# Performance work log

Hardware: AMD Instinct MI355X
Metric: run time of the kernel (lower is better)

## Reference

```python
import jax, jax.numpy as jnp
import numpy as np

EMBED_DIM = 1024
NUM_HEADS = 8
SEQ_LEN = 2048
EPS = 1e-6


def setup_inputs() -> dict:
    key = jax.random.key(0)
    ks = jax.random.split(key, 8)
    E, NH, S = EMBED_DIM, NUM_HEADS, SEQ_LEN
    q = jax.random.normal(ks[0], (S, E), jnp.float32)
    k = jax.random.normal(ks[1], (S, E), jnp.float32)
    v = jax.random.normal(ks[2], (S, E), jnp.float32)
    # gate projections: weights init'd to zeros in the module; use small random
    # values so the gate math is exercised. Biases follow the module's init.
    Wi = 0.02 * jax.random.normal(ks[3], (NH, 3 * E), jnp.float32)
    bi = jnp.linspace(3.0, 6.0, NH, dtype=jnp.float32)
    Wf = 0.02 * jax.random.normal(ks[4], (NH, 3 * E), jnp.float32)
    bf = jnp.sqrt(0.1) * jax.random.normal(ks[5], (NH,), jnp.float32)
    # ResidualLayerNorm (xLSTM-style): effective scale = 1 + weight, no bias
    ln_weight = jnp.zeros((E,), jnp.float32)
    return {"q": q, "k": k, "v": v, "Wi": Wi, "bi": bi, "Wf": Wf, "bf": bf,
            "ln_weight": ln_weight}


def _mlstm_parallel(q, k, v, Wi, bi, Wf, bf, ln_weight):
    S, E = q.shape
    NH = Wi.shape[0]
    DH = E // NH
    gate_in = jnp.concatenate((q, k, v), axis=1)            # (S, 3E)
    ig = (gate_in @ Wi.T + bi).T[:, :, None]                # (NH, S, 1)
    fg = (gate_in @ Wf.T + bf).T[:, :, None]                # (NH, S, 1)

    qh = q.reshape(S, NH, DH).transpose(1, 0, 2)            # (NH, S, DH)
    kh = k.reshape(S, NH, DH).transpose(1, 0, 2)
    vh = v.reshape(S, NH, DH).transpose(1, 0, 2)

    # cumulative log forget gates
    log_f = jax.nn.log_sigmoid(fg)                          # (NH, S, 1)
    log_f_cum = jnp.concatenate(
        [jnp.zeros((NH, 1, 1), q.dtype), jnp.cumsum(log_f, axis=1)], axis=1
    )                                                       # (NH, S+1, 1)
    log_fg_mat = log_f_cum - log_f_cum.transpose(0, 2, 1)   # (NH, S+1, S+1)
    causal = jnp.tril(jnp.ones((S, S), bool))
    log_fg_mat = jnp.where(causal, log_fg_mat[:, 1:, 1:], -jnp.inf)  # (NH,S,S)

    log_D = log_fg_mat + ig.transpose(0, 2, 1)              # (NH, S, S)
    max_log_D = jnp.max(log_D, axis=-1, keepdims=True)      # (NH, S, 1)
    D = jnp.exp(log_D - max_log_D)                          # stabilized

    qk = jnp.einsum('hsd,htd->hst', qh, kh) / jnp.sqrt(jnp.asarray(DH, q.dtype))
    C = qk * D                                              # (NH, S, S)
    normalizer = jnp.maximum(jnp.abs(jnp.sum(C, axis=-1, keepdims=True)),
                             jnp.exp(-max_log_D))
    C_norm = C / (normalizer + EPS)
    h = jnp.einsum('hst,htd->hsd', C_norm, vh)              # (NH, S, DH)
    h = h.transpose(1, 0, 2).reshape(S, E)

    # residual layer norm: LN(h) * (1 + weight), no bias
    mu = jnp.mean(h, axis=-1, keepdims=True)
    var = jnp.mean(jnp.square(h - mu), axis=-1, keepdims=True)
    h_norm = (h - mu) * jax.lax.rsqrt(var + 1e-5)
    return h_norm * (1.0 + ln_weight)


def reference(q, k, v, Wi, bi, Wf, bf, ln_weight):
    return _mlstm_parallel(q, k, v, Wi, bi, Wf, bf, ln_weight)
```

## Files before the change

kernel.cpp:

```cpp
#include <hip/hip_runtime.h>
#include <math.h>

#define S_LEN 2048
#define EMB   1024
#define NHEAD 8
#define DH    128
#define E3    3072
#define BM    64
#define BN    32
#define NSPLIT 4
#define KSTRIDE  136
#define VTSTRIDE 40
#define PTSTRIDE 40

typedef __bf16 bf16x8 __attribute__((ext_vector_type(8)));
typedef __bf16 bf16x4 __attribute__((ext_vector_type(4)));
typedef float  f32x4  __attribute__((ext_vector_type(4)));

__global__ __launch_bounds__(256) void gates_cvt_transpose_kernel(
    const float* __restrict__ q, const float* __restrict__ k,
    const float* __restrict__ v,
    const float* __restrict__ Wi, const float* __restrict__ bi,
    const float* __restrict__ Wf, const float* __restrict__ bf,
    __bf16* __restrict__ Qh, __bf16* __restrict__ Ql,
    __bf16* __restrict__ Kh, __bf16* __restrict__ Kl,
    __bf16* __restrict__ Vt,
    float* __restrict__ ig, float* __restrict__ lf)
{
    const int tid = threadIdx.x;
    __shared__ union {
        float red[16][4];
        __bf16 tile[32][33];
    } sh;

    if (blockIdx.x < S_LEN) {
        const int t = blockIdx.x;
        const float4 qv = ((const float4*)q)[(size_t)t * 256 + tid];
        const float4 kv = ((const float4*)k)[(size_t)t * 256 + tid];
        const float4 vv = ((const float4*)v)[(size_t)t * 256 + tid];
        {
            size_t idx = (size_t)t * 256 + tid;
            bf16x4 hi, lo;
            hi[0]=(__bf16)qv.x; hi[1]=(__bf16)qv.y; hi[2]=(__bf16)qv.z; hi[3]=(__bf16)qv.w;
            lo[0]=(__bf16)(qv.x-(float)hi[0]); lo[1]=(__bf16)(qv.y-(float)hi[1]);
            lo[2]=(__bf16)(qv.z-(float)hi[2]); lo[3]=(__bf16)(qv.w-(float)hi[3]);
            ((bf16x4*)Qh)[idx] = hi; ((bf16x4*)Ql)[idx] = lo;
            hi[0]=(__bf16)kv.x; hi[1]=(__bf16)kv.y; hi[2]=(__bf16)kv.z; hi[3]=(__bf16)kv.w;
            lo[0]=(__bf16)(kv.x-(float)hi[0]); lo[1]=(__bf16)(kv.y-(float)hi[1]);
            lo[2]=(__bf16)(kv.z-(float)hi[2]); lo[3]=(__bf16)(kv.w-(float)hi[3]);
            ((bf16x4*)Kh)[idx] = hi; ((bf16x4*)Kl)[idx] = lo;
        }
        float acc[16];
        #pragma unroll
        for (int g = 0; g < 16; ++g) {
            const float4* w4 = (const float4*)((g < 8) ? (Wi + g * E3) : (Wf + (g - 8) * E3));
            float4 a = w4[tid], b = w4[256 + tid], c = w4[512 + tid];
            acc[g] = a.x*qv.x + a.y*qv.y + a.z*qv.z + a.w*qv.w
                   + b.x*kv.x + b.y*kv.y + b.z*kv.z + b.w*kv.w
                   + c.x*vv.x + c.y*vv.y + c.z*vv.z + c.w*vv.w;
        }
        const int w = tid >> 6, lane = tid & 63;
        #pragma unroll
        for (int g = 0; g < 16; ++g) {
            float x = acc[g];
            for (int o = 32; o > 0; o >>= 1) x += __shfl_down(x, o, 64);
            if (lane == 0) sh.red[g][w] = x;
        }
        __syncthreads();
        if (tid < 16) {
            float s = sh.red[tid][0] + sh.red[tid][1] + sh.red[tid][2] + sh.red[tid][3];
            if (tid < 8) {
                ig[tid * S_LEN + t] = s + bi[tid];
            } else {
                int h = tid - 8;
                float x = s + bf[h];
                lf[h * S_LEN + t] = fminf(x, 0.f) - log1pf(expf(-fabsf(x)));
            }
        }
    } else {
        const int tb = blockIdx.x - S_LEN;
        const int sb = (tb & 63) * 32, eb = (tb >> 6) * 32;
        #pragma unroll
        for (int i = 0; i < 4; ++i) {
            int lin = tid + i * 256;
            int sr = lin >> 5, ec = lin & 31;
            sh.tile[ec][sr] = (__bf16)v[(size_t)(sb + sr) * EMB + eb + ec];
        }
        __syncthreads();
        #pragma unroll
        for (int i = 0; i < 4; ++i) {
            int lin = tid + i * 256;
            int er = lin >> 5, sc = lin & 31;
            Vt[(size_t)(eb + er) * S_LEN + sb + sc] = sh.tile[er][sc];
        }
    }
}

__global__ __launch_bounds__(256) void cumsum_aux_kernel(
    const float* __restrict__ lf, const float* __restrict__ ig,
    float* __restrict__ F, float* __restrict__ ug,
    float* __restrict__ umax, float* __restrict__ upmax)
{
    const int h = blockIdx.x, tid = threadIdx.x;
    __shared__ float ssum[256];
    __shared__ float morig[256];
    float loc[8];
    const int base = tid * 8;
    float s = 0.f;
    for (int i = 0; i < 8; i++) { s += lf[h * S_LEN + base + i]; loc[i] = s; }
    ssum[tid] = s;
    __syncthreads();
    for (int o = 1; o < 256; o <<= 1) {
        float add = (tid >= o) ? ssum[tid - o] : 0.f;
        __syncthreads();
        ssum[tid] += add;
        __syncthreads();
    }
    float prev = (tid > 0) ? ssum[tid - 1] : 0.f;
    float* Fh = F + h * (S_LEN + 1);
    if (tid == 0) Fh[0] = 0.f;
    float Fv[8];
    for (int i = 0; i < 8; i++) { Fv[i] = prev + loc[i]; Fh[base + i + 1] = Fv[i]; }

    const float* igh = ig + h * S_LEN;
    float pm[8];
    float runm = -1e30f;
    #pragma unroll
    for (int i = 0; i < 8; i++) {
        float u = igh[base + i] - Fv[i];
        ug[h * S_LEN + base + i] = u;
        runm = fmaxf(runm, u);
        pm[i] = runm;
    }
    morig[tid] = runm;
    __syncthreads();
    const int g0 = tid & ~3;
    float pfx = -1e30f;
    for (int j = g0; j < tid; ++j) pfx = fmaxf(pfx, morig[j]);
    #pragma unroll
    for (int i = 0; i < 8; i++)
        upmax[h * S_LEN + base + i] = fmaxf(pfx, pm[i]);
    if ((tid & 3) == 0) {
        float mm = fmaxf(fmaxf(morig[tid], morig[tid + 1]),
                         fmaxf(morig[tid + 2], morig[tid + 3]));
        umax[h * 64 + (tid >> 2)] = mm;
    }
}

__global__ __launch_bounds__(256, 2) void mlstm_mfma(
    const __bf16* __restrict__ Qhg, const __bf16* __restrict__ Qlg,
    const __bf16* __restrict__ Khg, const __bf16* __restrict__ Klg,
    const __bf16* __restrict__ Vtg,
    const float* __restrict__ ug, const float* __restrict__ umaxg,
    const float* __restrict__ upmaxg, const float* __restrict__ F,
    __bf16* __restrict__ Opart, float* __restrict__ msplit,
    float* __restrict__ lsplit)
{
    const int flat = blockIdx.x;
    const int h = flat & 7;
    const int rest = flat >> 3;
    const int xx = rest & 15, z = rest >> 4;
    const int tid  = threadIdx.x;
    const int lane = tid & 63, w = tid >> 6;
    const int quad = lane >> 4, l15 = lane & 15;

    __shared__ __bf16 Kh[BN * KSTRIDE], Kl[BN * KSTRIDE];
    __shared__ __bf16 Vt[DH * VTSTRIDE];
    __shared__ __bf16 Pt[4][16 * PTSTRIDE];

    const float* Fh  = F  + h * (S_LEN + 1);
    const float* ugh = ug + h * S_LEN;
    const float scale = 0.088388347648318447f;
    const int kr  = tid >> 4, kc8 = tid & 15;
    const int vr0 = tid >> 2, vc0 = tid & 3;

    for (int pair = 0; pair < 2; ++pair) {
        const int qt = (pair == 0) ? xx : 31 - xx;
        const int qb = qt * BM;
        const int nj = 2 * qt + 2;
        const int j0 = (z * nj) / NSPLIT, j1 = ((z + 1) * nj) / NSPLIT;

        float fq[4], upm[4];
        int sglob[4], sblk[4];
        #pragma unroll
        for (int r = 0; r < 4; ++r) {
            int s = qb + w * 16 + quad * 4 + r;
            sglob[r] = s; sblk[r] = s >> 5;
            fq[r]  = Fh[s + 1];
            upm[r] = upmaxg[h * S_LEN + s];
        }
        float m_r[4] = {-1e30f, -1e30f, -1e30f, -1e30f};
        float l_r[4] = {0.f, 0.f, 0.f, 0.f};
        f32x4 Oacc[8] = {{0,0,0,0},{0,0,0,0},{0,0,0,0},{0,0,0,0},
                         {0,0,0,0},{0,0,0,0},{0,0,0,0},{0,0,0,0}};

        bf16x8 pk[2], pl[2], pv[2];
        if (j0 < j1) {
            const int tb = j0 * BN;
            #pragma unroll
            for (int i = 0; i < 2; ++i) {
                int row = kr + 16 * i;
                size_t g = (size_t)(tb + row) * EMB + h * DH + kc8 * 8;
                pk[i] = *(const bf16x8*)(Khg + g);
                pl[i] = *(const bf16x8*)(Klg + g);
                pv[i] = *(const bf16x8*)(Vtg + (size_t)(h * DH + vr0 + 64 * i) * S_LEN + tb + vc0 * 8);
            }
        }

        for (int j = j0; j < j1; ++j) {
            const int tb = j * BN;
            __syncthreads();
            #pragma unroll
            for (int i = 0; i < 2; ++i) {
                int row = kr + 16 * i;
                *(bf16x8*)&Kh[row * KSTRIDE + kc8 * 8] = pk[i];
                *(bf16x8*)&Kl[row * KSTRIDE + kc8 * 8] = pl[i];
                *(bf16x8*)&Vt[(vr0 + 64 * i) * VTSTRIDE + vc0 * 8] = pv[i];
            }
            __syncthreads();
            if (j + 1 < j1) {
                const int tb2 = tb + BN;
                #pragma unroll
                for (int i = 0; i < 2; ++i) {
                    int row = kr + 16 * i;
                    size_t g = (size_t)(tb2 + row) * EMB + h * DH + kc8 * 8;
                    pk[i] = *(const bf16x8*)(Khg + g);
                    pl[i] = *(const bf16x8*)(Klg + g);
                    pv[i] = *(const bf16x8*)(Vtg + (size_t)(h * DH + vr0 + 64 * i) * S_LEN + tb2 + vc0 * 8);
                }
            }
            bf16x8 qh[4], ql[4];
            {
                const size_t qrow = (size_t)(qb + w * 16 + l15) * EMB + h * DH + quad * 8;
                #pragma unroll
                for (int kk = 0; kk < 4; ++kk) {
                    qh[kk] = *(const bf16x8*)(Qhg + qrow + kk * 32);
                    ql[kk] = *(const bf16x8*)(Qlg + qrow + kk * 32);
                }
            }
            f32x4 S0 = {0,0,0,0}, S1 = {0,0,0,0};
            #pragma unroll
            for (int kk = 0; kk < 4; ++kk) {
                const int co = kk * 32 + quad * 8;
                bf16x8 bh0 = *(const bf16x8*)&Kh[l15 * KSTRIDE + co];
                bf16x8 bl0 = *(const bf16x8*)&Kl[l15 * KSTRIDE + co];
                S0 = __builtin_amdgcn_mfma_f32_16x16x32_bf16(qh[kk], bh0, S0, 0, 0, 0);
                S0 = __builtin_amdgcn_mfma_f32_16x16x32_bf16(qh[kk], bl0, S0, 0, 0, 0);
                S0 = __builtin_amdgcn_mfma_f32_16x16x32_bf16(ql[kk], bh0, S0, 0, 0, 0);
                bf16x8 bh1 = *(const bf16x8*)&Kh[(16 + l15) * KSTRIDE + co];
                bf16x8 bl1 = *(const bf16x8*)&Kl[(16 + l15) * KSTRIDE + co];
                S1 = __builtin_amdgcn_mfma_f32_16x16x32_bf16(qh[kk], bh1, S1, 0, 0, 0);
                S1 = __builtin_amdgcn_mfma_f32_16x16x32_bf16(qh[kk], bl1, S1, 0, 0, 0);
                S1 = __builtin_amdgcn_mfma_f32_16x16x32_bf16(ql[kk], bh1, S1, 0, 0, 0);
            }
            const int t0 = tb + l15, t1 = tb + 16 + l15;
            const float ut0 = ugh[t0], ut1 = ugh[t1];
            const float umj = umaxg[h * 64 + j];
            #pragma unroll
            for (int r = 0; r < 4; ++r) {
                float mt = (j < sblk[r]) ? (fq[r] + umj)
                         : (j == sblk[r]) ? (fq[r] + upm[r]) : -1e30f;
                float mn = fmaxf(m_r[r], mt);
                float alpha = __expf(m_r[r] - mn);
                m_r[r] = mn;
                l_r[r] *= alpha;
                #pragma unroll
                for (int nt = 0; nt < 8; ++nt) Oacc[nt][r] *= alpha;
                float p0 = __expf(fq[r] + ut0 - mn) * S0[r] * scale;
                float p1 = __expf(fq[r] + ut1 - mn) * S1[r] * scale;
                if (j >= sblk[r]) {
                    if (t0 > sglob[r]) p0 = 0.f;
                    if (t1 > sglob[r]) p1 = 0.f;
                }
                float x = p0 + p1;
                #pragma unroll
                for (int o = 1; o < 16; o <<= 1) x += __shfl_xor(x, o);
                l_r[r] += x;
                const int prow = (quad * 4 + r) * PTSTRIDE;
                Pt[w][prow + l15]      = (__bf16)p0;
                Pt[w][prow + 16 + l15] = (__bf16)p1;
            }
            bf16x8 pa = *(const bf16x8*)&Pt[w][l15 * PTSTRIDE + quad * 8];
            #pragma unroll
            for (int nt = 0; nt < 8; ++nt) {
                bf16x8 vb = *(const bf16x8*)&Vt[(nt * 16 + l15) * VTSTRIDE + quad * 8];
                Oacc[nt] = __builtin_amdgcn_mfma_f32_16x16x32_bf16(pa, vb, Oacc[nt], 0, 0, 0);
            }
        }
        __bf16* Oz = Opart + (size_t)z * S_LEN * EMB;
        #pragma unroll
        for (int nt = 0; nt < 8; ++nt) {
            #pragma unroll
            for (int r = 0; r < 4; ++r) {
                Oz[(size_t)sglob[r] * EMB + h * DH + nt * 16 + l15] = (__bf16)Oacc[nt][r];
            }
        }
        if (l15 == 0) {
            #pragma unroll
            for (int r = 0; r < 4; ++r) {
                msplit[(z * NHEAD + h) * S_LEN + sglob[r]] = m_r[r];
                lsplit[(z * NHEAD + h) * S_LEN + sglob[r]] = l_r[r];
            }
        }
    }
}

__global__ __launch_bounds__(256) void combine_ln_kernel(
    const __bf16* __restrict__ Opart, const float* __restrict__ msplit,
    const float* __restrict__ lsplit, const float* __restrict__ lnw,
    float* __restrict__ out)
{
    const int s = blockIdx.x, tid = threadIdx.x;
    __shared__ float es_s[NSPLIT][NHEAD];
    __shared__ float rn_s[NHEAD];
    __shared__ float red[4];
    if (tid < NHEAD) {
        float mz[NSPLIT], lz[NSPLIT];
        float m = -1e30f;
        #pragma unroll
        for (int zz = 0; zz < NSPLIT; ++zz) {
            mz[zz] = msplit[(zz * NHEAD + tid) * S_LEN + s];
            lz[zz] = lsplit[(zz * NHEAD + tid) * S_LEN + s];
            m = fmaxf(m, mz[zz]);
        }
        float l = 0.f;
        #pragma unroll
        for (int zz = 0; zz < NSPLIT; ++zz) {
            float e = __expf(mz[zz] - m);
            es_s[zz][tid] = e;
            l += e * lz[zz];
        }
        rn_s[tid] = 1.f / (fmaxf(fabsf(l), __expf(-m)) + 1e-6f);
    }
    __syncthreads();
    const size_t SE = (size_t)S_LEN * EMB;
    float x[4];
    float sum = 0.f;
    #pragma unroll
    for (int i = 0; i < 4; i++) {
        int col = tid + i * 256;
        int hh = col >> 7;
        size_t off = (size_t)s * EMB + col;
        float val = 0.f;
        #pragma unroll
        for (int zz = 0; zz < NSPLIT; ++zz)
            val += es_s[zz][hh] * (float)Opart[zz * SE + off];
        x[i] = val * rn_s[hh];
        sum += x[i];
    }
    for (int o = 32; o > 0; o >>= 1) sum += __shfl_down(sum, o, 64);
    if ((tid & 63) == 0) red[tid >> 6] = sum;
    __syncthreads();
    sum = red[0] + red[1] + red[2] + red[3];
    const float mu = sum * (1.f / EMB);
    float vs = 0.f;
    #pragma unroll
    for (int i = 0; i < 4; i++) { float d = x[i] - mu; vs += d * d; }
    __syncthreads();
    for (int o = 32; o > 0; o >>= 1) vs += __shfl_down(vs, o, 64);
    if ((tid & 63) == 0) red[tid >> 6] = vs;
    __syncthreads();
    vs = red[0] + red[1] + red[2] + red[3];
    const float rstd = rsqrtf(vs * (1.f / EMB) + 1e-5f);
    #pragma unroll
    for (int i = 0; i < 4; i++) {
        int c = tid + i * 256;
        out[(size_t)s * EMB + c] = (x[i] - mu) * rstd * (1.f + lnw[c]);
    }
}

extern "C" void kernel_launch(void* const* d_in, const int* in_sizes, int n_in,
                              void* d_out, int out_size, void* d_ws, size_t ws_size,
                              hipStream_t stream)
{
    const float* q   = (const float*)d_in[0];
    const float* k   = (const float*)d_in[1];
    const float* v   = (const float*)d_in[2];
    const float* Wi  = (const float*)d_in[3];
    const float* bi  = (const float*)d_in[4];
    const float* Wf  = (const float*)d_in[5];
    const float* bf  = (const float*)d_in[6];
    const float* lnw = (const float*)d_in[7];
    float* out = (float*)d_out;

    float* ws = (float*)d_ws;
    float* ig    = ws;
    float* lf    = ig + NHEAD * S_LEN;
    float* F     = lf + NHEAD * S_LEN;
    float* ugw   = F + NHEAD * (S_LEN + 1);
    float* umaxw = ugw + NHEAD * S_LEN;
    float* upmaxw= umaxw + NHEAD * 64;
    __bf16* Qh = (__bf16*)(upmaxw + NHEAD * S_LEN);
    const size_t SEb = (size_t)S_LEN * EMB;
    __bf16* Ql  = Qh + SEb;
    __bf16* Kh  = Ql + SEb;
    __bf16* Kl  = Kh + SEb;
    __bf16* Vtg = Kl + SEb;
    __bf16* Opart = Vtg + SEb;
    float* msplit = (float*)(Opart + (size_t)NSPLIT * SEb);
    float* lsplit = msplit + NSPLIT * NHEAD * S_LEN;

    gates_cvt_transpose_kernel<<<2 * S_LEN, 256, 0, stream>>>(
        q, k, v, Wi, bi, Wf, bf, Qh, Ql, Kh, Kl, Vtg, ig, lf);
    cumsum_aux_kernel<<<NHEAD, 256, 0, stream>>>(lf, ig, F, ugw, umaxw, upmaxw);
    mlstm_mfma<<<16 * NHEAD * NSPLIT, 256, 0, stream>>>(
        Qh, Ql, Kh, Kl, Vtg, ugw, umaxw, upmaxw, F, Opart, msplit, lsplit);
    combine_ln_kernel<<<S_LEN, 256, 0, stream>>>(Opart, msplit, lsplit, lnw, out);
}
```

Measured before the change: 159.9 us.

## Unpair query tiles into separate blocks, raise occupancy, vectorize combine kernel

The attention kernel stops processing a paired (short, long) query tile per block and instead launches one block per query tile, doubling the grid, with the launch bound raised to 4 blocks per CU. The combine/layernorm kernel now handles two rows per block with 8 contiguous columns per thread, using bf16x8 and float4 vector loads and stores, and computes per-head merge weights per thread instead of through shared memory. The goal is more parallelism and latency hiding in the main kernel and fewer, wider memory transactions in the combine. The cost is that the causal work is no longer balanced across blocks, and the tighter register budget may cause spills.

```diff
diff --git a/kernel.cpp b/kernel.cpp
--- a/kernel.cpp
+++ b/kernel.cpp
@@ -147,7 +147,7 @@
     }
 }
 
-__global__ __launch_bounds__(256, 2) void mlstm_mfma(
+__global__ __launch_bounds__(256, 4) void mlstm_mfma(
     const __bf16* __restrict__ Qhg, const __bf16* __restrict__ Qlg,
     const __bf16* __restrict__ Khg, const __bf16* __restrict__ Klg,
     const __bf16* __restrict__ Vtg,
@@ -157,9 +157,9 @@
     float* __restrict__ lsplit)
 {
     const int flat = blockIdx.x;
-    const int h = flat & 7;
-    const int rest = flat >> 3;
-    const int xx = rest & 15, z = rest >> 4;
+    const int h  = flat & 7;
+    const int qt = (flat >> 3) & 31;
+    const int z  = flat >> 8;
     const int tid  = threadIdx.x;
     const int lane = tid & 63, w = tid >> 6;
     const int quad = lane >> 4, l15 = lane & 15;
@@ -174,133 +174,130 @@
     const int kr  = tid >> 4, kc8 = tid & 15;
     const int vr0 = tid >> 2, vc0 = tid & 3;
 
-    for (int pair = 0; pair < 2; ++pair) {
-        const int qt = (pair == 0) ? xx : 31 - xx;
-        const int qb = qt * BM;
-        const int nj = 2 * qt + 2;
-        const int j0 = (z * nj) / NSPLIT, j1 = ((z + 1) * nj) / NSPLIT;
-
-        float fq[4], upm[4];
-        int sglob[4], sblk[4];
-        #pragma unroll
-        for (int r = 0; r < 4; ++r) {
-            int s = qb + w * 16 + quad * 4 + r;
-            sglob[r] = s; sblk[r] = s >> 5;
-            fq[r]  = Fh[s + 1];
-            upm[r] = upmaxg[h * S_LEN + s];
-        }
-        float m_r[4] = {-1e30f, -1e30f, -1e30f, -1e30f};
-        float l_r[4] = {0.f, 0.f, 0.f, 0.f};
-        f32x4 Oacc[8] = {{0,0,0,0},{0,0,0,0},{0,0,0,0},{0,0,0,0},
-                         {0,0,0,0},{0,0,0,0},{0,0,0,0},{0,0,0,0}};
-
-        bf16x8 pk[2], pl[2], pv[2];
-        if (j0 < j1) {
-            const int tb = j0 * BN;
+    const int qb = qt * BM;
+    const int nj = 2 * qt + 2;
+    const int j0 = (z * nj) / NSPLIT, j1 = ((z + 1) * nj) / NSPLIT;
+
+    float fq[4], upm[4];
+    int sglob[4], sblk[4];
+    #pragma unroll
+    for (int r = 0; r < 4; ++r) {
+        int s = qb + w * 16 + quad * 4 + r;
+        sglob[r] = s; sblk[r] = s >> 5;
+        fq[r]  = Fh[s + 1];
+        upm[r] = upmaxg[h * S_LEN + s];
+    }
+    float m_r[4] = {-1e30f, -1e30f, -1e30f, -1e30f};
+    float l_r[4] = {0.f, 0.f, 0.f, 0.f};
+    f32x4 Oacc[8] = {{0,0,0,0},{0,0,0,0},{0,0,0,0},{0,0,0,0},
+                     {0,0,0,0},{0,0,0,0},{0,0,0,0},{0,0,0,0}};
+
+    bf16x8 pk[2], pl[2], pv[2];
+    if (j0 < j1) {
+        const int tb = j0 * BN;
+        #pragma unroll
+        for (int i = 0; i < 2; ++i) {
+            int row = kr + 16 * i;
+            size_t g = (size_t)(tb + row) * EMB + h * DH + kc8 * 8;
+            pk[i] = *(const bf16x8*)(Khg + g);
+            pl[i] = *(const bf16x8*)(Klg + g);
+            pv[i] = *(const bf16x8*)(Vtg + (size_t)(h * DH + vr0 + 64 * i) * S_LEN + tb + vc0 * 8);
+        }
+    }
+
+    for (int j = j0; j < j1; ++j) {
+        const int tb = j * BN;
+        __syncthreads();
+        #pragma unroll
+        for (int i = 0; i < 2; ++i) {
+            int row = kr + 16 * i;
+            *(bf16x8*)&Kh[row * KSTRIDE + kc8 * 8] = pk[i];
+            *(bf16x8*)&Kl[row * KSTRIDE + kc8 * 8] = pl[i];
+            *(bf16x8*)&Vt[(vr0 + 64 * i) * VTSTRIDE + vc0 * 8] = pv[i];
+        }
+        __syncthreads();
+        if (j + 1 < j1) {
+            const int tb2 = tb + BN;
             #pragma unroll
             for (int i = 0; i < 2; ++i) {
                 int row = kr + 16 * i;
-                size_t g = (size_t)(tb + row) * EMB + h * DH + kc8 * 8;
+                size_t g = (size_t)(tb2 + row) * EMB + h * DH + kc8 * 8;
                 pk[i] = *(const bf16x8*)(Khg + g);
                 pl[i] = *(const bf16x8*)(Klg + g);
-                pv[i] = *(const bf16x8*)(Vtg + (size_t)(h * DH + vr0 + 64 * i) * S_LEN + tb + vc0 * 8);
+                pv[i] = *(const bf16x8*)(Vtg + (size_t)(h * DH + vr0 + 64 * i) * S_LEN + tb2 + vc0 * 8);
             }
         }
-
-        for (int j = j0; j < j1; ++j) {
-            const int tb = j * BN;
-            __syncthreads();
-            #pragma unroll
-            for (int i = 0; i < 2; ++i) {
-                int row = kr + 16 * i;
-                *(bf16x8*)&Kh[row * KSTRIDE + kc8 * 8] = pk[i];
-                *(bf16x8*)&Kl[row * KSTRIDE + kc8 * 8] = pl[i];
-                *(bf16x8*)&Vt[(vr0 + 64 * i) * VTSTRIDE + vc0 * 8] = pv[i];
-            }
-            __syncthreads();
-            if (j + 1 < j1) {
-                const int tb2 = tb + BN;
-                #pragma unroll
-                for (int i = 0; i < 2; ++i) {
-                    int row = kr + 16 * i;
-                    size_t g = (size_t)(tb2 + row) * EMB + h * DH + kc8 * 8;
-                    pk[i] = *(const bf16x8*)(Khg + g);
-                    pl[i] = *(const bf16x8*)(Klg + g);
-                    pv[i] = *(const bf16x8*)(Vtg + (size_t)(h * DH + vr0 + 64 * i) * S_LEN + tb2 + vc0 * 8);
-                }
-            }
-            bf16x8 qh[4], ql[4];
-            {
-                const size_t qrow = (size_t)(qb + w * 16 + l15) * EMB + h * DH + quad * 8;
-                #pragma unroll
-                for (int kk = 0; kk < 4; ++kk) {
-                    qh[kk] = *(const bf16x8*)(Qhg + qrow + kk * 32);
-                    ql[kk] = *(const bf16x8*)(Qlg + qrow + kk * 32);
-                }
-            }
-            f32x4 S0 = {0,0,0,0}, S1 = {0,0,0,0};
+        bf16x8 qh[4], ql[4];
+        {
+            const size_t qrow = (size_t)(qb + w * 16 + l15) * EMB + h * DH + quad * 8;
             #pragma unroll
             for (int kk = 0; kk < 4; ++kk) {
-                const int co = kk * 32 + quad * 8;
-                bf16x8 bh0 = *(const bf16x8*)&Kh[l15 * KSTRIDE + co];
-                bf16x8 bl0 = *(const bf16x8*)&Kl[l15 * KSTRIDE + co];
-                S0 = __builtin_amdgcn_mfma_f32_16x16x32_bf16(qh[kk], bh0, S0, 0, 0, 0);
-                S0 = __builtin_amdgcn_mfma_f32_16x16x32_bf16(qh[kk], bl0, S0, 0, 0, 0);
-                S0 = __builtin_amdgcn_mfma_f32_16x16x32_bf16(ql[kk], bh0, S0, 0, 0, 0);
-                bf16x8 bh1 = *(const bf16x8*)&Kh[(16 + l15) * KSTRIDE + co];
-                bf16x8 bl1 = *(const bf16x8*)&Kl[(16 + l15) * KSTRIDE + co];
-                S1 = __builtin_amdgcn_mfma_f32_16x16x32_bf16(qh[kk], bh1, S1, 0, 0, 0);
-                S1 = __builtin_amdgcn_mfma_f32_16x16x32_bf16(qh[kk], bl1, S1, 0, 0, 0);
-                S1 = __builtin_amdgcn_mfma_f32_16x16x32_bf16(ql[kk], bh1, S1, 0, 0, 0);
+                qh[kk] = *(const bf16x8*)(Qhg + qrow + kk * 32);
+                ql[kk] = *(const bf16x8*)(Qlg + qrow + kk * 32);
             }
-            const int t0 = tb + l15, t1 = tb + 16 + l15;
-            const float ut0 = ugh[t0], ut1 = ugh[t1];
-            const float umj = umaxg[h * 64 + j];
+        }
+        f32x4 S0 = {0,0,0,0}, S1 = {0,0,0,0};
+        #pragma unroll
+        for (int kk = 0; kk < 4; ++kk) {
+            const int co = kk * 32 + quad * 8;
+            bf16x8 bh0 = *(const bf16x8*)&Kh[l15 * KSTRIDE + co];
+            bf16x8 bl0 = *(const bf16x8*)&Kl[l15 * KSTRIDE + co];
+            S0 = __builtin_amdgcn_mfma_f32_16x16x32_bf16(qh[kk], bh0, S0, 0, 0, 0);
+            S0 = __builtin_amdgcn_mfma_f32_16x16x32_bf16(qh[kk], bl0, S0, 0, 0, 0);
+            S0 = __builtin_amdgcn_mfma_f32_16x16x32_bf16(ql[kk], bh0, S0, 0, 0, 0);
+            bf16x8 bh1 = *(const bf16x8*)&Kh[(16 + l15) * KSTRIDE + co];
+            bf16x8 bl1 = *(const bf16x8*)&Kl[(16 + l15) * KSTRIDE + co];
+            S1 = __builtin_amdgcn_mfma_f32_16x16x32_bf16(qh[kk], bh1, S1, 0, 0, 0);
+            S1 = __builtin_amdgcn_mfma_f32_16x16x32_bf16(qh[kk], bl1, S1, 0, 0, 0);
+            S1 = __builtin_amdgcn_mfma_f32_16x16x32_bf16(ql[kk], bh1, S1, 0, 0, 0);
+        }
+        const int t0 = tb + l15, t1 = tb + 16 + l15;
+        const float ut0 = ugh[t0], ut1 = ugh[t1];
+        const float umj = umaxg[h * 64 + j];
+        #pragma unroll
+        for (int r = 0; r < 4; ++r) {
+            float mt = (j < sblk[r]) ? (fq[r] + umj)
+                     : (j == sblk[r]) ? (fq[r] + upm[r]) : -1e30f;
+            float mn = fmaxf(m_r[r], mt);
+            float alpha = __expf(m_r[r] - mn);
+            m_r[r] = mn;
+            l_r[r] *= alpha;
             #pragma unroll
-            for (int r = 0; r < 4; ++r) {
-                float mt = (j < sblk[r]) ? (fq[r] + umj)
-                         : (j == sblk[r]) ? (fq[r] + upm[r]) : -1e30f;
-                float mn = fmaxf(m_r[r], mt);
-                float alpha = __expf(m_r[r] - mn);
-                m_r[r] = mn;
-                l_r[r] *= alpha;
-                #pragma unroll
-                for (int nt = 0; nt < 8; ++nt) Oacc[nt][r] *= alpha;
-                float p0 = __expf(fq[r] + ut0 - mn) * S0[r] * scale;
-                float p1 = __expf(fq[r] + ut1 - mn) * S1[r] * scale;
-                if (j >= sblk[r]) {
-                    if (t0 > sglob[r]) p0 = 0.f;
-                    if (t1 > sglob[r]) p1 = 0.f;
-                }
-                float x = p0 + p1;
-                #pragma unroll
-                for (int o = 1; o < 16; o <<= 1) x += __shfl_xor(x, o);
-                l_r[r] += x;
-                const int prow = (quad * 4 + r) * PTSTRIDE;
-                Pt[w][prow + l15]      = (__bf16)p0;
-                Pt[w][prow + 16 + l15] = (__bf16)p1;
+            for (int nt = 0; nt < 8; ++nt) Oacc[nt][r] *= alpha;
+            float p0 = __expf(fq[r] + ut0 - mn) * S0[r] * scale;
+            float p1 = __expf(fq[r] + ut1 - mn) * S1[r] * scale;
+            if (j >= sblk[r]) {
+                if (t0 > sglob[r]) p0 = 0.f;
+                if (t1 > sglob[r]) p1 = 0.f;
             }
-            bf16x8 pa = *(const bf16x8*)&Pt[w][l15 * PTSTRIDE + quad * 8];
+            float x = p0 + p1;
             #pragma unroll
-            for (int nt = 0; nt < 8; ++nt) {
-                bf16x8 vb = *(const bf16x8*)&Vt[(nt * 16 + l15) * VTSTRIDE + quad * 8];
-                Oacc[nt] = __builtin_amdgcn_mfma_f32_16x16x32_bf16(pa, vb, Oacc[nt], 0, 0, 0);
-            }
-        }
-        __bf16* Oz = Opart + (size_t)z * S_LEN * EMB;
+            for (int o = 1; o < 16; o <<= 1) x += __shfl_xor(x, o);
+            l_r[r] += x;
+            const int prow = (quad * 4 + r) * PTSTRIDE;
+            Pt[w][prow + l15]      = (__bf16)p0;
+            Pt[w][prow + 16 + l15] = (__bf16)p1;
+        }
+        bf16x8 pa = *(const bf16x8*)&Pt[w][l15 * PTSTRIDE + quad * 8];
         #pragma unroll
         for (int nt = 0; nt < 8; ++nt) {
-            #pragma unroll
-            for (int r = 0; r < 4; ++r) {
-                Oz[(size_t)sglob[r] * EMB + h * DH + nt * 16 + l15] = (__bf16)Oacc[nt][r];
-            }
-        }
-        if (l15 == 0) {
-            #pragma unroll
-            for (int r = 0; r < 4; ++r) {
-                msplit[(z * NHEAD + h) * S_LEN + sglob[r]] = m_r[r];
-                lsplit[(z * NHEAD + h) * S_LEN + sglob[r]] = l_r[r];
-            }
+            bf16x8 vb = *(const bf16x8*)&Vt[(nt * 16 + l15) * VTSTRIDE + quad * 8];
+            Oacc[nt] = __builtin_amdgcn_mfma_f32_16x16x32_bf16(pa, vb, Oacc[nt], 0, 0, 0);
+        }
+    }
+    __bf16* Oz = Opart + (size_t)z * S_LEN * EMB;
+    #pragma unroll
+    for (int nt = 0; nt < 8; ++nt) {
+        #pragma unroll
+        for (int r = 0; r < 4; ++r) {
+            Oz[(size_t)sglob[r] * EMB + h * DH + nt * 16 + l15] = (__bf16)Oacc[nt][r];
+        }
+    }
+    if (l15 == 0) {
+        #pragma unroll
+        for (int r = 0; r < 4; ++r) {
+            msplit[(z * NHEAD + h) * S_LEN + sglob[r]] = m_r[r];
+            lsplit[(z * NHEAD + h) * S_LEN + sglob[r]] = l_r[r];
         }
     }
 }
@@ -310,63 +307,58 @@
     const float* __restrict__ lsplit, const float* __restrict__ lnw,
     float* __restrict__ out)
 {
-    const int s = blockIdx.x, tid = threadIdx.x;
-    __shared__ float es_s[NSPLIT][NHEAD];
-    __shared__ float rn_s[NHEAD];
-    __shared__ float red[4];
-    if (tid < NHEAD) {
-        float mz[NSPLIT], lz[NSPLIT];
-        float m = -1e30f;
-        #pragma unroll
-        for (int zz = 0; zz < NSPLIT; ++zz) {
-            mz[zz] = msplit[(zz * NHEAD + tid) * S_LEN + s];
-            lz[zz] = lsplit[(zz * NHEAD + tid) * S_LEN + s];
-            m = fmaxf(m, mz[zz]);
-        }
-        float l = 0.f;
-        #pragma unroll
-        for (int zz = 0; zz < NSPLIT; ++zz) {
-            float e = __expf(mz[zz] - m);
-            es_s[zz][tid] = e;
-            l += e * lz[zz];
-        }
-        rn_s[tid] = 1.f / (fmaxf(fabsf(l), __expf(-m)) + 1e-6f);
-    }
+    const int tid = threadIdx.x;
+    const int r  = tid >> 7;
+    const int wr = (tid >> 6) & 1;
+    const int c0 = (tid & 127) * 8;
+    const int hh = c0 >> 7;
+    const int s  = blockIdx.x * 2 + r;
+    __shared__ float redsum[2][2], redvar[2][2];
+
+    float m = -1e30f, es[NSPLIT], l = 0.f;
+    #pragma unroll
+    for (int zz = 0; zz < NSPLIT; ++zz)
+        m = fmaxf(m, msplit[(zz * NHEAD + hh) * S_LEN + s]);
+    #pragma unroll
+    for (int zz = 0; zz < NSPLIT; ++zz) {
+        es[zz] = __expf(msplit[(zz * NHEAD + hh) * S_LEN + s] - m);
+        l += es[zz] * lsplit[(zz * NHEAD + hh) * S_LEN + s];
+    }
+    const float rn = 1.f / (fmaxf(fabsf(l), __expf(-m)) + 1e-6f);
+
+    const size_t SE = (size_t)S_LEN * EMB;
+    float x[8] = {0,0,0,0,0,0,0,0};
+    #pragma unroll
+    for (int zz = 0; zz < NSPLIT; ++zz) {
+        bf16x8 o = *(const bf16x8*)(Opart + zz * SE + (size_t)s * EMB + c0);
+        #pragma unroll
+        for (int e = 0; e < 8; ++e) x[e] += es[zz] * (float)o[e];
+    }
+    float sum = 0.f;
+    #pragma unroll
+    for (int e = 0; e < 8; ++e) { x[e] *= rn; sum += x[e]; }
+    for (int o = 32; o > 0; o >>= 1) sum += __shfl_down(sum, o, 64);
+    if ((tid & 63) == 0) redsum[r][wr] = sum;
     __syncthreads();
-    const size_t SE = (size_t)S_LEN * EMB;
-    float x[4];
-    float sum = 0.f;
-    #pragma unroll
-    for (int i = 0; i < 4; i++) {
-        int col = tid + i * 256;
-        int hh = col >> 7;
-        size_t off = (size_t)s * EMB + col;
-        float val = 0.f;
-        #pragma unroll
-        for (int zz = 0; zz < NSPLIT; ++zz)
-            val += es_s[zz][hh] * (float)Opart[zz * SE + off];
-        x[i] = val * rn_s[hh];
-        sum += x[i];
-    }
-    for (int o = 32; o > 0; o >>= 1) sum += __shfl_down(sum, o, 64);
-    if ((tid & 63) == 0) red[tid >> 6] = sum;
-    __syncthreads();
-    sum = red[0] + red[1] + red[2] + red[3];
+    sum = redsum[r][0] + redsum[r][1];
     const float mu = sum * (1.f / EMB);
     float vs = 0.f;
     #pragma unroll
-    for (int i = 0; i < 4; i++) { float d = x[i] - mu; vs += d * d; }
+    for (int e = 0; e < 8; ++e) { float d = x[e] - mu; vs += d * d; }
+    for (int o = 32; o > 0; o >>= 1) vs += __shfl_down(vs, o, 64);
+    if ((tid & 63) == 0) redvar[r][wr] = vs;
     __syncthreads();
-    for (int o = 32; o > 0; o >>= 1) vs += __shfl_down(vs, o, 64);
-    if ((tid & 63) == 0) red[tid >> 6] = vs;
-    __syncthreads();
-    vs = red[0] + red[1] + red[2] + red[3];
+    vs = redvar[r][0] + redvar[r][1];
     const float rstd = rsqrtf(vs * (1.f / EMB) + 1e-5f);
-    #pragma unroll
-    for (int i = 0; i < 4; i++) {
-        int c = tid + i * 256;
-        out[(size_t)s * EMB + c] = (x[i] - mu) * rstd * (1.f + lnw[c]);
-    }
+    const float4 w0 = *(const float4*)(lnw + c0);
+    const float4 w1 = *(const float4*)(lnw + c0 + 4);
+    float4 o0, o1;
+    o0.x = (x[0]-mu)*rstd*(1.f+w0.x); o0.y = (x[1]-mu)*rstd*(1.f+w0.y);
+    o0.z = (x[2]-mu)*rstd*(1.f+w0.z); o0.w = (x[3]-mu)*rstd*(1.f+w0.w);
+    o1.x = (x[4]-mu)*rstd*(1.f+w1.x); o1.y = (x[5]-mu)*rstd*(1.f+w1.y);
+    o1.z = (x[6]-mu)*rstd*(1.f+w1.z); o1.w = (x[7]-mu)*rstd*(1.f+w1.w);
+    *(float4*)(out + (size_t)s * EMB + c0)     = o0;
+    *(float4*)(out + (size_t)s * EMB + c0 + 4) = o1;
 }
 
 extern "C" void kernel_launch(void* const* d_in, const int* in_sizes, int n_in,
@@ -403,7 +395,7 @@
     gates_cvt_transpose_kernel<<<2 * S_LEN, 256, 0, stream>>>(
         q, k, v, Wi, bi, Wf, bf, Qh, Ql, Kh, Kl, Vtg, ig, lf);
     cumsum_aux_kernel<<<NHEAD, 256, 0, stream>>>(lf, ig, F, ugw, umaxw, upmaxw);
-    mlstm_mfma<<<16 * NHEAD * NSPLIT, 256, 0, stream>>>(
+    mlstm_mfma<<<32 * NHEAD * NSPLIT, 256, 0, stream>>>(
         Qh, Ql, Kh, Kl, Vtg, ugw, umaxw, upmaxw, F, Opart, msplit, lsplit);
-    combine_ln_kernel<<<S_LEN, 256, 0, stream>>>(Opart, msplit, lsplit, lnw, out);
+    combine_ln_kernel<<<S_LEN / 2, 256, 0, stream>>>(Opart, msplit, lsplit, lnw, out);
 }
```

Result: slower. 238.3 us (+49.0%).
